# Kernel tuning notes

Measured on AMD Instinct MI355X. Metric: run time of the kernel, lower is better.

## Reference

```python
import jax, jax.numpy as jnp
import numpy as np

B = 524288
IN_A = 32
IN_S = 32
D = IN_A + IN_S      # combined expert input
E = 8                # num_experts
H = 64               # expert_hidden_size
GH = 32              # gating_hidden_size


def setup_inputs() -> dict:
    key = jax.random.key(0)
    ks = jax.random.split(key, 10)
    s = 0.05
    return {
        "A_data": jax.random.normal(ks[0], (B, IN_A), jnp.float32),
        "S_data": jax.random.normal(ks[1], (B, IN_S), jnp.float32),
        # gating MLP (in=IN_S -> GH -> E), weights stored as [in, out]
        "gate_w1": jax.random.normal(ks[2], (IN_S, GH), jnp.float32) * s,
        "gate_b1": jnp.zeros((GH,), jnp.float32),
        "gate_w2": jax.random.normal(ks[3], (GH, E), jnp.float32) * s,
        "gate_b2": jnp.zeros((E,), jnp.float32),
        # E expert MLPs (in=D -> H -> 1), batched over expert dim
        "exp_w1": jax.random.normal(ks[4], (E, D, H), jnp.float32) * s,
        "exp_b1": jnp.zeros((E, H), jnp.float32),
        "exp_w2": jax.random.normal(ks[5], (E, H), jnp.float32) * s,  # out=1, squeezed
        "exp_b2": jnp.zeros((E,), jnp.float32),
    }


def reference(A_data, S_data, gate_w1, gate_b1, gate_w2, gate_b2,
              exp_w1, exp_b1, exp_w2, exp_b2):
    # gating: MLP(S) -> softmax over experts
    gh = jax.nn.relu(S_data @ gate_w1 + gate_b1)                    # [B, GH]
    gating_probs = jax.nn.softmax(gh @ gate_w2 + gate_b2, axis=1)   # [B, E]
    # all experts on full batch (dense ensemble)
    x = jnp.concatenate([A_data, S_data], axis=-1)                  # [B, D]
    eh = jax.nn.relu(jnp.einsum("bd,edh->beh", x, exp_w1) + exp_b1) # [B, E, H]
    eo = jnp.einsum("beh,eh->be", eh, exp_w2) + exp_b2              # [B, E]
    # weighted sum over experts, keepdim -> [B, 1]
    return jnp.sum(eo * gating_probs, axis=1, keepdims=True)
```

## Files before the change

### kernel.cpp

```cpp
#include <hip/hip_runtime.h>
#include <hip/hip_bf16.h>
#include <math.h>

#define ROWS 256
#define DD 64
#define EE 8
#define HH 64
#define GHD 32

typedef __attribute__((ext_vector_type(8))) short bf16x8;
typedef __attribute__((ext_vector_type(4))) float f32x4;

static __device__ __forceinline__ short f2bf(float f) {
    unsigned u = __builtin_bit_cast(unsigned, f);
    unsigned r = (u + 0x7fffu + ((u >> 16) & 1u)) >> 16;
    return (short)r;
}
static __device__ __forceinline__ unsigned pk2(float lo, float hi) {
    __hip_bfloat162 h = __float22bfloat162_rn(make_float2(lo, hi));
    unsigned r;
    __builtin_memcpy(&r, &h, 4);
    return r;
}
template <int CTRL>
static __device__ __forceinline__ float dpp_add(float x) {
    int xi = __builtin_bit_cast(int, x);
    int yi = __builtin_amdgcn_update_dpp(0, xi, CTRL, 0xF, 0xF, true);
    return x + __builtin_bit_cast(float, yi);
}
static __device__ __forceinline__ float bperm_add(float x, int addr) {
    int xi = __builtin_bit_cast(int, x);
    int yi = __builtin_amdgcn_ds_bpermute(addr, xi);
    return x + __builtin_bit_cast(float, yi);
}

__global__ __launch_bounds__(256) void prep_kernel(const float* __restrict__ ew1,
                                                   const float* __restrict__ gw1,
                                                   short* __restrict__ wf) {
    int idx = blockIdx.x * 256 + threadIdx.x;
    int lane = idx & 63;
    int half = (idx >> 6) & 1;
    int tt   = (idx >> 7) & 7;
    int wave = (idx >> 10) & 3;
    int n = wave * 128 + tt * 16 + (lane & 15);
    int e = n >> 6, h = n & 63;
    int quad = lane >> 4;
    short v[8];
    #pragma unroll
    for (int j = 0; j < 8; ++j) {
        int dl = quad * 8 + j + half * 32;
        v[j] = f2bf(ew1[(e * DD + dl) * HH + h]);
    }
    *(bf16x8*)(wf + (size_t)idx * 8) = *(const bf16x8*)v;
    if (idx < 128) {
        int tile = idx >> 6;
        int lr = lane & 15;
        short g[8];
        #pragma unroll
        for (int j = 0; j < 8; ++j)
            g[j] = f2bf(gw1[(quad * 8 + j) * GHD + tile * 16 + lr]);
        *(bf16x8*)(wf + 32768 + (size_t)idx * 8) = *(const bf16x8*)g;
    }
}

__global__ __launch_bounds__(256, 3) void moe_kernel(
    const float* __restrict__ A, const float* __restrict__ S,
    const float* __restrict__ gb1, const float* __restrict__ gw2,
    const float* __restrict__ gb2, const short* __restrict__ wf,
    const float* __restrict__ eb1, const float* __restrict__ ew2,
    const float* __restrict__ eb2, float* __restrict__ out)
{
    __shared__ __align__(16) short xs[ROWS][72];
    __shared__ __align__(16) float ps[ROWS][EE];
    __shared__ __align__(16) float ghs[4][16][36];

    const int t = threadIdx.x;
    const int row0 = blockIdx.x * ROWS;
    const int lane = t & 63;
    const int wave = t >> 6;
    const int quad = lane >> 4;
    const int lr = lane & 15;

    {
        const int row = row0 + t;
        const float4* ar = (const float4*)(A + (size_t)row * 32);
        const float4* sr = (const float4*)(S + (size_t)row * 32);
        #pragma unroll
        for (int i = 0; i < 4; ++i) {
            float4 v0 = ar[2 * i], v1 = ar[2 * i + 1];
            uint4 u;
            u.x = pk2(v0.x, v0.y); u.y = pk2(v0.z, v0.w);
            u.z = pk2(v1.x, v1.y); u.w = pk2(v1.z, v1.w);
            *(uint4*)&xs[t][i * 8] = u;
        }
        #pragma unroll
        for (int i = 0; i < 4; ++i) {
            float4 v0 = sr[2 * i], v1 = sr[2 * i + 1];
            uint4 u;
            u.x = pk2(v0.x, v0.y); u.y = pk2(v0.z, v0.w);
            u.z = pk2(v1.x, v1.y); u.w = pk2(v1.z, v1.w);
            *(uint4*)&xs[t][32 + i * 8] = u;
        }
    }
    asm volatile("s_waitcnt lgkmcnt(0)" ::: "memory");
    __builtin_amdgcn_sched_barrier(0);

    {
        const short* gwf = wf + 32768;
        bf16x8 gf0 = *(const bf16x8*)(gwf + (size_t)lane * 8);
        bf16x8 gf1 = *(const bf16x8*)(gwf + 512 + (size_t)lane * 8);
        float gw2r[8][8];
        #pragma unroll
        for (int j = 0; j < 8; ++j) {
            float4 a0 = *(const float4*)(gw2 + (quad * 8 + j) * 8);
            float4 a1 = *(const float4*)(gw2 + (quad * 8 + j) * 8 + 4);
            gw2r[j][0] = a0.x; gw2r[j][1] = a0.y; gw2r[j][2] = a0.z; gw2r[j][3] = a0.w;
            gw2r[j][4] = a1.x; gw2r[j][5] = a1.y; gw2r[j][6] = a1.z; gw2r[j][7] = a1.w;
        }
        const float gb1v0 = gb1[lr], gb1v1 = gb1[lr + 16];
        float gb2v[8];
        #pragma unroll
        for (int e = 0; e < 8; ++e) gb2v[e] = gb2[e];
        const int a16 = (lane ^ 16) << 2;
        const int a32 = (lane ^ 32) << 2;

        #pragma unroll 1
        for (int i = 0; i < 4; ++i) {
            const int rt = wave * 4 + i;
            bf16x8 sa = *(const bf16x8*)&xs[rt * 16 + lr][32 + quad * 8];
            f32x4 acc0 = {gb1v0, gb1v0, gb1v0, gb1v0};
            f32x4 acc1 = {gb1v1, gb1v1, gb1v1, gb1v1};
            acc0 = __builtin_amdgcn_mfma_f32_16x16x32_bf16(sa, gf0, acc0, 0, 0, 0);
            acc1 = __builtin_amdgcn_mfma_f32_16x16x32_bf16(sa, gf1, acc1, 0, 0, 0);
            #pragma unroll
            for (int r = 0; r < 4; ++r) {
                ghs[wave][quad * 4 + r][lr]      = fmaxf(acc0[r], 0.f);
                ghs[wave][quad * 4 + r][lr + 16] = fmaxf(acc1[r], 0.f);
            }
            asm volatile("s_waitcnt lgkmcnt(0)" ::: "memory");
            __builtin_amdgcn_sched_barrier(0);
            f32x4 g0 = *(const f32x4*)&ghs[wave][lr][quad * 8];
            f32x4 g1 = *(const f32x4*)&ghs[wave][lr][quad * 8 + 4];
            float lg[8];
            #pragma unroll
            for (int e = 0; e < 8; ++e) lg[e] = 0.f;
            #pragma unroll
            for (int j = 0; j < 4; ++j) {
                #pragma unroll
                for (int e = 0; e < 8; ++e) lg[e] = fmaf(g0[j], gw2r[j][e], lg[e]);
            }
            #pragma unroll
            for (int j = 0; j < 4; ++j) {
                #pragma unroll
                for (int e = 0; e < 8; ++e) lg[e] = fmaf(g1[j], gw2r[4 + j][e], lg[e]);
            }
            #pragma unroll
            for (int e = 0; e < 8; ++e) {
                float v = bperm_add(lg[e], a16);
                v = bperm_add(v, a32);
                lg[e] = v + gb2v[e];
            }
            float mx = fmaxf(fmaxf(fmaxf(lg[0], lg[1]), fmaxf(lg[2], lg[3])),
                             fmaxf(fmaxf(lg[4], lg[5]), fmaxf(lg[6], lg[7])));
            float pv[8], sum = 0.f;
            #pragma unroll
            for (int e = 0; e < 8; ++e) { pv[e] = __expf(lg[e] - mx); sum += pv[e]; }
            const float inv = __builtin_amdgcn_rcpf(sum);
            if (quad == 0) {
                float4 p0 = make_float4(pv[0] * inv, pv[1] * inv, pv[2] * inv, pv[3] * inv);
                float4 p1 = make_float4(pv[4] * inv, pv[5] * inv, pv[6] * inv, pv[7] * inv);
                *(float4*)&ps[rt * 16 + lr][0] = p0;
                *(float4*)&ps[rt * 16 + lr][4] = p1;
            }
        }
    }

    bf16x8 blo[8], bhi[8];
    float w2p[8], b1c[8];
    const int e0 = wave * 2;
    #pragma unroll
    for (int tt = 0; tt < 8; ++tt) {
        const short* base = wf + ((size_t)((wave * 8 + tt) * 128) + lane) * 8;
        blo[tt] = *(const bf16x8*)base;
        bhi[tt] = *(const bf16x8*)(base + 512);
        int n = wave * 128 + tt * 16 + lr;
        int e = n >> 6, h = n & 63;
        w2p[tt] = ew2[e * HH + h];
        b1c[tt] = eb1[e * HH + h];
    }
    const float ebi0 = eb2[e0] * 0.0625f;
    const float ebi1 = eb2[e0 + 1] * 0.0625f;

    __syncthreads();

    #pragma unroll 1
    for (int rt = 0; rt < ROWS / 16; ++rt) {
        const short* xp = &xs[rt * 16 + lr][quad * 8];
        bf16x8 alo = *(const bf16x8*)xp;
        bf16x8 ahi = *(const bf16x8*)(xp + 32);
        f32x4 acc[8];
        #pragma unroll
        for (int tt = 0; tt < 8; ++tt)
            acc[tt] = (f32x4){b1c[tt], b1c[tt], b1c[tt], b1c[tt]};
        #pragma unroll
        for (int tt = 0; tt < 8; ++tt)
            acc[tt] = __builtin_amdgcn_mfma_f32_16x16x32_bf16(alo, blo[tt], acc[tt], 0, 0, 0);
        #pragma unroll
        for (int tt = 0; tt < 8; ++tt)
            acc[tt] = __builtin_amdgcn_mfma_f32_16x16x32_bf16(ahi, bhi[tt], acc[tt], 0, 0, 0);

        float pe0[4] = {ebi0, ebi0, ebi0, ebi0};
        float pe1[4] = {ebi1, ebi1, ebi1, ebi1};
        #pragma unroll
        for (int tt = 0; tt < 8; ++tt) {
            #pragma unroll
            for (int r = 0; r < 4; ++r) {
                float v = fmaxf(acc[tt][r], 0.0f);
                if (tt < 4) pe0[r] = fmaf(v, w2p[tt], pe0[r]);
                else        pe1[r] = fmaf(v, w2p[tt], pe1[r]);
            }
        }
        #pragma unroll
        for (int r = 0; r < 4; ++r) {
            const int rw = rt * 16 + quad * 4 + r;
            float c = fmaf(pe0[r], ps[rw][e0], pe1[r] * ps[rw][e0 + 1]);
            c = dpp_add<0xB1>(c);
            c = dpp_add<0x4E>(c);
            c = dpp_add<0x124>(c);
            c = dpp_add<0x128>(c);
            if (lr == 0) *(float*)&xs[rw][64 + 2 * wave] = c;
        }
    }

    __syncthreads();
    const float4 fs = *(const float4*)&xs[t][64];
    out[row0 + t] = (fs.x + fs.y) + (fs.z + fs.w);
}

extern "C" void kernel_launch(void* const* d_in, const int* in_sizes, int n_in,
                              void* d_out, int out_size, void* d_ws, size_t ws_size,
                              hipStream_t stream) {
    const float* A   = (const float*)d_in[0];
    const float* S   = (const float*)d_in[1];
    const float* gw1 = (const float*)d_in[2];
    const float* gb1 = (const float*)d_in[3];
    const float* gw2 = (const float*)d_in[4];
    const float* gb2 = (const float*)d_in[5];
    const float* ew1 = (const float*)d_in[6];
    const float* eb1 = (const float*)d_in[7];
    const float* ew2 = (const float*)d_in[8];
    const float* eb2 = (const float*)d_in[9];
    float* out = (float*)d_out;
    short* wf = (short*)d_ws;

    const int B = in_sizes[0] / 32;
    hipLaunchKernelGGL(prep_kernel, dim3(16), dim3(256), 0, stream, ew1, gw1, wf);
    hipLaunchKernelGGL(moe_kernel, dim3(B / ROWS), dim3(256), 0, stream,
                       A, S, gb1, gw2, gb2, wf, eb1, ew2, eb2, out);
}
```

Baseline: 205.8 us.

## Keep gating hidden in registers, store probs as bf16, raise occupancy to 4

Swaps the gating MFMA operand order so each lane holds hidden units for its own row. The second gating layer is then computed directly from MFMA accumulators, without the LDS round trip and wait through the ghs buffer. Gating probabilities are stored in LDS as bf16 instead of fp32, and launch bounds are raised to 4 blocks per CU. Together these cut LDS use and traffic to allow more resident blocks. The trade-offs are lower precision in the gating weights and possible register pressure or spilling under the tighter per-thread register budget.

```diff
diff --git a/kernel.cpp b/kernel.cpp
--- a/kernel.cpp
+++ b/kernel.cpp
@@ -15,6 +15,10 @@
     unsigned u = __builtin_bit_cast(unsigned, f);
     unsigned r = (u + 0x7fffu + ((u >> 16) & 1u)) >> 16;
     return (short)r;
+}
+static __device__ __forceinline__ float bf2f(unsigned short b) {
+    unsigned u = ((unsigned)b) << 16;
+    return __builtin_bit_cast(float, u);
 }
 static __device__ __forceinline__ unsigned pk2(float lo, float hi) {
     __hip_bfloat162 h = __float22bfloat162_rn(make_float2(lo, hi));
@@ -63,7 +67,7 @@
     }
 }
 
-__global__ __launch_bounds__(256, 3) void moe_kernel(
+__global__ __launch_bounds__(256, 4) void moe_kernel(
     const float* __restrict__ A, const float* __restrict__ S,
     const float* __restrict__ gb1, const float* __restrict__ gw2,
     const float* __restrict__ gb2, const short* __restrict__ wf,
@@ -71,8 +75,7 @@
     const float* __restrict__ eb2, float* __restrict__ out)
 {
     __shared__ __align__(16) short xs[ROWS][72];
-    __shared__ __align__(16) float ps[ROWS][EE];
-    __shared__ __align__(16) float ghs[4][16][36];
+    __shared__ __align__(16) unsigned short psb[ROWS][EE];
 
     const int t = threadIdx.x;
     const int row0 = blockIdx.x * ROWS;
@@ -111,13 +114,18 @@
         bf16x8 gf1 = *(const bf16x8*)(gwf + 512 + (size_t)lane * 8);
         float gw2r[8][8];
         #pragma unroll
-        for (int j = 0; j < 8; ++j) {
-            float4 a0 = *(const float4*)(gw2 + (quad * 8 + j) * 8);
-            float4 a1 = *(const float4*)(gw2 + (quad * 8 + j) * 8 + 4);
+        for (int j = 0; j < 4; ++j) {
+            float4 a0 = *(const float4*)(gw2 + (quad * 4 + j) * 8);
+            float4 a1 = *(const float4*)(gw2 + (quad * 4 + j) * 8 + 4);
             gw2r[j][0] = a0.x; gw2r[j][1] = a0.y; gw2r[j][2] = a0.z; gw2r[j][3] = a0.w;
             gw2r[j][4] = a1.x; gw2r[j][5] = a1.y; gw2r[j][6] = a1.z; gw2r[j][7] = a1.w;
-        }
-        const float gb1v0 = gb1[lr], gb1v1 = gb1[lr + 16];
+            float4 b0 = *(const float4*)(gw2 + (16 + quad * 4 + j) * 8);
+            float4 b1 = *(const float4*)(gw2 + (16 + quad * 4 + j) * 8 + 4);
+            gw2r[4 + j][0] = b0.x; gw2r[4 + j][1] = b0.y; gw2r[4 + j][2] = b0.z; gw2r[4 + j][3] = b0.w;
+            gw2r[4 + j][4] = b1.x; gw2r[4 + j][5] = b1.y; gw2r[4 + j][6] = b1.z; gw2r[4 + j][7] = b1.w;
+        }
+        const f32x4 binit0 = *(const f32x4*)(gb1 + quad * 4);
+        const f32x4 binit1 = *(const f32x4*)(gb1 + 16 + quad * 4);
         float gb2v[8];
         #pragma unroll
         for (int e = 0; e < 8; ++e) gb2v[e] = gb2[e];
@@ -127,32 +135,24 @@
         #pragma unroll 1
         for (int i = 0; i < 4; ++i) {
             const int rt = wave * 4 + i;
-            bf16x8 sa = *(const bf16x8*)&xs[rt * 16 + lr][32 + quad * 8];
-            f32x4 acc0 = {gb1v0, gb1v0, gb1v0, gb1v0};
-            f32x4 acc1 = {gb1v1, gb1v1, gb1v1, gb1v1};
-            acc0 = __builtin_amdgcn_mfma_f32_16x16x32_bf16(sa, gf0, acc0, 0, 0, 0);
-            acc1 = __builtin_amdgcn_mfma_f32_16x16x32_bf16(sa, gf1, acc1, 0, 0, 0);
+            bf16x8 sb = *(const bf16x8*)&xs[rt * 16 + lr][32 + quad * 8];
+            f32x4 acc0 = binit0, acc1 = binit1;
+            acc0 = __builtin_amdgcn_mfma_f32_16x16x32_bf16(gf0, sb, acc0, 0, 0, 0);
+            acc1 = __builtin_amdgcn_mfma_f32_16x16x32_bf16(gf1, sb, acc1, 0, 0, 0);
+            float lg[8];
+            #pragma unroll
+            for (int e = 0; e < 8; ++e) lg[e] = 0.f;
             #pragma unroll
             for (int r = 0; r < 4; ++r) {
-                ghs[wave][quad * 4 + r][lr]      = fmaxf(acc0[r], 0.f);
-                ghs[wave][quad * 4 + r][lr + 16] = fmaxf(acc1[r], 0.f);
-            }
-            asm volatile("s_waitcnt lgkmcnt(0)" ::: "memory");
-            __builtin_amdgcn_sched_barrier(0);
-            f32x4 g0 = *(const f32x4*)&ghs[wave][lr][quad * 8];
-            f32x4 g1 = *(const f32x4*)&ghs[wave][lr][quad * 8 + 4];
-            float lg[8];
-            #pragma unroll
-            for (int e = 0; e < 8; ++e) lg[e] = 0.f;
-            #pragma unroll
-            for (int j = 0; j < 4; ++j) {
+                float v = fmaxf(acc0[r], 0.f);
                 #pragma unroll
-                for (int e = 0; e < 8; ++e) lg[e] = fmaf(g0[j], gw2r[j][e], lg[e]);
-            }
-            #pragma unroll
-            for (int j = 0; j < 4; ++j) {
+                for (int e = 0; e < 8; ++e) lg[e] = fmaf(v, gw2r[r][e], lg[e]);
+            }
+            #pragma unroll
+            for (int r = 0; r < 4; ++r) {
+                float v = fmaxf(acc1[r], 0.f);
                 #pragma unroll
-                for (int e = 0; e < 8; ++e) lg[e] = fmaf(g1[j], gw2r[4 + j][e], lg[e]);
+                for (int e = 0; e < 8; ++e) lg[e] = fmaf(v, gw2r[4 + r][e], lg[e]);
             }
             #pragma unroll
             for (int e = 0; e < 8; ++e) {
@@ -167,10 +167,12 @@
             for (int e = 0; e < 8; ++e) { pv[e] = __expf(lg[e] - mx); sum += pv[e]; }
             const float inv = __builtin_amdgcn_rcpf(sum);
             if (quad == 0) {
-                float4 p0 = make_float4(pv[0] * inv, pv[1] * inv, pv[2] * inv, pv[3] * inv);
-                float4 p1 = make_float4(pv[4] * inv, pv[5] * inv, pv[6] * inv, pv[7] * inv);
-                *(float4*)&ps[rt * 16 + lr][0] = p0;
-                *(float4*)&ps[rt * 16 + lr][4] = p1;
+                uint4 u;
+                u.x = pk2(pv[0] * inv, pv[1] * inv);
+                u.y = pk2(pv[2] * inv, pv[3] * inv);
+                u.z = pk2(pv[4] * inv, pv[5] * inv);
+                u.w = pk2(pv[6] * inv, pv[7] * inv);
+                *(uint4*)&psb[rt * 16 + lr][0] = u;
             }
         }
     }
@@ -223,7 +225,7 @@
         #pragma unroll
         for (int r = 0; r < 4; ++r) {
             const int rw = rt * 16 + quad * 4 + r;
-            float c = fmaf(pe0[r], ps[rw][e0], pe1[r] * ps[rw][e0 + 1]);
+            float c = fmaf(pe0[r], bf2f(psb[rw][e0]), pe1[r] * bf2f(psb[rw][e0 + 1]));
             c = dpp_add<0xB1>(c);
             c = dpp_add<0x4E>(c);
             c = dpp_add<0x124>(c);
```

Result: slower. 293.6 us (+42.7%).
